# Performance work log

Measured on AMD Instinct MI355X. Metric: run time of the kernel, lower is better.

The kernel has to match this reference:

```python
import jax, jax.numpy as jnp
import numpy as np

TBL_V = 1000      # table_id_vocab
IDX_V = 100000    # idx_id_vocab
D     = 128       # embed_dim
T_OUT = 8         # output_length
BLK   = 2048      # block_size
H     = 8         # n_heads
L     = 2         # n_layers
DFF   = 2048      # nn.TransformerEncoderLayer default dim_feedforward
HID   = 4 * D     # hidden_dim
B, S  = 128, 200
NSEG  = IDX_V // BLK + 1   # 49 segment tables
EPS   = 1e-5


def setup_inputs() -> dict:
    key = jax.random.key(0)
    ks = iter(jax.random.split(key, 48))
    def n(shape, s=0.02):
        return jax.random.normal(next(ks), shape, jnp.float32) * s
    return {
        "table_id_seq": jax.random.randint(next(ks), (B, S), 0, TBL_V, jnp.int32),
        "idx_id_seq":   jax.random.randint(next(ks), (B, S), 0, IDX_V, jnp.int32),
        # embedding tables (idx tables stacked: segment s occupies rows [s*BLK,(s+1)*BLK))
        "table_embed": n((TBL_V, D), 1.0),
        "idx_embed":   n((NSEG * BLK, D), 1.0),
        # two independent TransformerEncoders (axis 0: 0=table, 1=idx), L layers each
        "Wqkv": n((2, L, 3 * D, D)), "bqkv": jnp.zeros((2, L, 3 * D), jnp.float32),
        "Wo":   n((2, L, D, D)),     "bo":   jnp.zeros((2, L, D), jnp.float32),
        "ln1_g": jnp.ones((2, L, D), jnp.float32), "ln1_b": jnp.zeros((2, L, D), jnp.float32),
        "W1": n((2, L, DFF, D)), "b1": jnp.zeros((2, L, DFF), jnp.float32),
        "W2": n((2, L, D, DFF)), "b2": jnp.zeros((2, L, D), jnp.float32),
        "ln2_g": jnp.ones((2, L, D), jnp.float32), "ln2_b": jnp.zeros((2, L, D), jnp.float32),
        "Wlin": n((HID, 2 * D)), "blin": jnp.zeros((HID,), jnp.float32),
        "Wtab": n((TBL_V, HID + 1)), "btab": jnp.zeros((TBL_V,), jnp.float32),
        "Widx": n((IDX_V, HID + 1)), "bidx": jnp.zeros((IDX_V,), jnp.float32),
    }


def _ln(x, g, b):
    m = x.mean(-1, keepdims=True)
    v = ((x - m) ** 2).mean(-1, keepdims=True)
    return (x - m) / jnp.sqrt(v + EPS) * g + b


def _encoder(x, p):
    """Post-norm TransformerEncoder (PyTorch defaults, eval mode). x: [B,S,D]."""
    Wqkv, bqkv, Wo, bo, g1, be1, W1, bf1, W2, bf2, g2, be2 = p
    Bz, Sl, Dm = x.shape
    hd = Dm // H
    for l in range(L):
        qkv = x @ Wqkv[l].T + bqkv[l]
        q, k, v = jnp.split(qkv, 3, axis=-1)
        q = q.reshape(Bz, Sl, H, hd)
        k = k.reshape(Bz, Sl, H, hd)
        v = v.reshape(Bz, Sl, H, hd)
        att = jnp.einsum('bqhd,bkhd->bhqk', q, k) * (hd ** -0.5)
        att = jax.nn.softmax(att, axis=-1)
        o = jnp.einsum('bhqk,bkhd->bqhd', att, v).reshape(Bz, Sl, Dm)
        o = o @ Wo[l].T + bo[l]
        x = _ln(x + o, g1[l], be1[l])
        f = jax.nn.relu(x @ W1[l].T + bf1[l]) @ W2[l].T + bf2[l]
        x = _ln(x + f, g2[l], be2[l])
    return x


def reference(table_id_seq, idx_id_seq, table_embed, idx_embed,
              Wqkv, bqkv, Wo, bo, ln1_g, ln1_b, W1, b1, W2, b2, ln2_g, ln2_b,
              Wlin, blin, Wtab, btab, Widx, bidx):
    enc_p = (Wqkv, bqkv, Wo, bo, ln1_g, ln1_b, W1, b1, W2, b2, ln2_g, ln2_b)
    te = table_embed[table_id_seq]                    # [B,S,D]
    # segment-routed lookup: row (seg*BLK + local) of stacked tables == original id
    ie = idx_embed[idx_id_seq]                        # [B,S,D]
    te = _encoder(te, tuple(a[0] for a in enc_p))
    ie = _encoder(ie, tuple(a[1] for a in enc_p))
    h = jnp.concatenate([te.mean(axis=1), ie.mean(axis=1)], axis=-1)  # mean over seq
    h = jax.nn.relu(h @ Wlin.T + blin)                # [B,HID]
    t = jnp.arange(T_OUT, dtype=h.dtype)
    # projection of [hidden, t]: base term + t * (last weight column)
    tab = (h @ Wtab[:, :HID].T + btab)[:, None, :] + t[None, :, None] * Wtab[:, HID][None, None, :]
    idx = (h @ Widx[:, :HID].T + bidx)[:, None, :] + t[None, :, None] * Widx[:, HID][None, None, :]
    return tab.reshape(-1, TBL_V), idx.reshape(-1, IDX_V)
```

## Files before the change

kernel.cpp:

```cpp
#include <hip/hip_runtime.h>

typedef __bf16 bf16x8 __attribute__((ext_vector_type(8)));
typedef float floatx4 __attribute__((ext_vector_type(4)));

__device__ __forceinline__ float u2f(unsigned short u) {
  union { unsigned int i; float f; } v; v.i = ((unsigned int)u) << 16; return v.f;
}
__device__ __forceinline__ unsigned short f2b(float f) {
  union { float f; unsigned int i; } v; v.f = f;
  unsigned int r = (v.i + 0x7fffu + ((v.i >> 16) & 1u)) >> 16;
  return (unsigned short)r;
}

__device__ __forceinline__ void gl16(const void* g, void* l) {
  __builtin_amdgcn_global_load_lds(
      (const __attribute__((address_space(1))) unsigned int*)g,
      (__attribute__((address_space(3))) unsigned int*)l, 16, 0, 0);
}

#define FCH 18048
#define QCH 8832
#define OCH 18176

#define LDS_STRIDE 48

__global__ __launch_bounds__(256) void gemm_kernel(
    const unsigned short* __restrict__ A, int lda,
    const float* __restrict__ W, int ldw,
    const float* __restrict__ bias,
    unsigned short* __restrict__ outB, float* __restrict__ outF,
    int M, int N, int K, int ldc, int mode)
{
  __shared__ unsigned short As[128 * LDS_STRIDE];
  __shared__ unsigned short Bs[128 * LDS_STRIDE];

  const int tid  = threadIdx.x;
  const int m0   = blockIdx.y * 128;
  const int n0   = blockIdx.x * 128;
  const int wave = tid >> 6;
  const int lane = tid & 63;
  const int wm   = (wave >> 1) * 64;
  const int wn   = (wave & 1) * 64;
  const int lr   = lane & 15;
  const int lq   = lane >> 4;

  floatx4 acc[4][4];
#pragma unroll
  for (int i = 0; i < 4; i++)
#pragma unroll
    for (int j = 0; j < 4; j++)
      acc[i][j] = (floatx4){0.f, 0.f, 0.f, 0.f};

  for (int k0 = 0; k0 < K; k0 += 32) {
    __syncthreads();
#pragma unroll
    for (int i = 0; i < 2; i++) {
      int c   = tid + i * 256;
      int row = c >> 2;
      int k8  = (c & 3) * 8;
      uint4 val = {0u, 0u, 0u, 0u};
      if (m0 + row < M)
        val = *(const uint4*)(A + (size_t)(m0 + row) * lda + k0 + k8);
      *(uint4*)(&As[row * LDS_STRIDE + k8]) = val;
    }
#pragma unroll
    for (int i = 0; i < 4; i++) {
      int c   = tid + i * 256;
      int row = c >> 3;
      int k4  = (c & 7) * 4;
      float f0 = 0.f, f1 = 0.f, f2 = 0.f, f3 = 0.f;
      if (n0 + row < N) {
        const float* p = W + (size_t)(n0 + row) * ldw + k0 + k4;
        f0 = p[0]; f1 = p[1]; f2 = p[2]; f3 = p[3];
      }
      ushort4 pk;
      pk.x = f2b(f0); pk.y = f2b(f1); pk.z = f2b(f2); pk.w = f2b(f3);
      *(ushort4*)(&Bs[row * LDS_STRIDE + k4]) = pk;
    }
    __syncthreads();

    bf16x8 af[4], bfr[4];
#pragma unroll
    for (int t = 0; t < 4; t++) {
      af[t]  = *(const bf16x8*)(&As[(wm + t * 16 + lr) * LDS_STRIDE + lq * 8]);
      bfr[t] = *(const bf16x8*)(&Bs[(wn + t * 16 + lr) * LDS_STRIDE + lq * 8]);
    }
#pragma unroll
    for (int tm = 0; tm < 4; tm++)
#pragma unroll
      for (int tn = 0; tn < 4; tn++)
        acc[tm][tn] = __builtin_amdgcn_mfma_f32_16x16x32_bf16(
            af[tm], bfr[tn], acc[tm][tn], 0, 0, 0);
  }

#pragma unroll
  for (int tm = 0; tm < 4; tm++) {
#pragma unroll
    for (int tn = 0; tn < 4; tn++) {
      int gcol = n0 + wn + tn * 16 + lr;
      if (gcol >= N) continue;
      float bs = bias[gcol];
      if (mode == 2) {
        float wl = W[(size_t)gcol * ldw + K];
#pragma unroll
        for (int r = 0; r < 4; r++) {
          int grow = m0 + wm + tm * 16 + lq * 4 + r;
          float base = acc[tm][tn][r] + bs;
          float* op = outF + ((size_t)grow * 8) * (size_t)N + gcol;
#pragma unroll
          for (int t = 0; t < 8; t++)
            op[(size_t)t * N] = base + (float)t * wl;
        }
      } else {
#pragma unroll
        for (int r = 0; r < 4; r++) {
          int grow = m0 + wm + tm * 16 + lq * 4 + r;
          if (grow < M) {
            float v = acc[tm][tn][r] + bs;
            if (mode == 1) v = fmaxf(v, 0.f);
            outB[(size_t)grow * ldc + gcol] = f2b(v);
          }
        }
      }
    }
  }
}

#define QKSTR 40
#define PSTR  232

__global__ __launch_bounds__(256) void attn_kernel(
    const unsigned short* __restrict__ qkv, unsigned short* __restrict__ out)
{
  __shared__ __attribute__((aligned(16))) unsigned short qsh[208 * QKSTR];
  __shared__ __attribute__((aligned(16))) unsigned short ksh[208 * QKSTR];
  __shared__ __attribute__((aligned(16))) unsigned short vsh[16 * PSTR];
  __shared__ __attribute__((aligned(16))) unsigned short psh[4][16 * PSTR];

  const int bh   = blockIdx.x;
  const int b    = bh >> 3, h = bh & 7;
  const int tid  = threadIdx.x;
  const int wave = tid >> 6;
  const int lane = tid & 63;
  const int lr   = lane & 15;
  const int lq   = lane >> 4;
  const size_t rowbase = (size_t)b * 200;

  for (int i = tid; i < 208 * QKSTR / 2; i += 256) {
    ((unsigned int*)qsh)[i] = 0u;
    ((unsigned int*)ksh)[i] = 0u;
  }
  for (int i = tid; i < 16 * PSTR / 2; i += 256)
    ((unsigned int*)vsh)[i] = 0u;
  for (int i = tid; i < 4 * 16 * PSTR / 2; i += 256)
    ((unsigned int*)&psh[0][0])[i] = 0u;
  __syncthreads();

  for (int i = tid; i < 800; i += 256) {
    int s = i >> 2, d4 = (i & 3) * 4;
    const unsigned short* base = qkv + (rowbase + s) * 384 + h * 16 + d4;
    uint2 qv = *(const uint2*)(base);
    uint2 kv = *(const uint2*)(base + 128);
    uint2 vv = *(const uint2*)(base + 256);
    *(uint2*)&qsh[s * QKSTR + d4] = qv;
    *(uint2*)&ksh[s * QKSTR + d4] = kv;
    vsh[(d4 + 0) * PSTR + s] = (unsigned short)(vv.x & 0xffffu);
    vsh[(d4 + 1) * PSTR + s] = (unsigned short)(vv.x >> 16);
    vsh[(d4 + 2) * PSTR + s] = (unsigned short)(vv.y & 0xffffu);
    vsh[(d4 + 3) * PSTR + s] = (unsigned short)(vv.y >> 16);
  }
  __syncthreads();

  unsigned short* pw = &psh[wave][0];

  for (int t = wave; t < 13; t += 4) {
    const int q0 = t * 16;
    bf16x8 qf = *(const bf16x8*)&qsh[(q0 + lr) * QKSTR + lq * 8];

    floatx4 s[13];
#pragma unroll
    for (int c = 0; c < 13; c++) {
      bf16x8 kf = *(const bf16x8*)&ksh[(c * 16 + lr) * QKSTR + lq * 8];
      s[c] = __builtin_amdgcn_mfma_f32_16x16x32_bf16(
          qf, kf, (floatx4){0.f, 0.f, 0.f, 0.f}, 0, 0, 0);
    }

    float mx[4] = {-1e30f, -1e30f, -1e30f, -1e30f};
#pragma unroll
    for (int c = 0; c < 13; c++)
#pragma unroll
      for (int r = 0; r < 4; r++) {
        float v = s[c][r] * 0.25f;
        if (c == 12 && lr >= 8) v = -1e30f;
        s[c][r] = v;
        mx[r] = fmaxf(mx[r], v);
      }
#pragma unroll
    for (int m = 1; m < 16; m <<= 1)
#pragma unroll
      for (int r = 0; r < 4; r++)
        mx[r] = fmaxf(mx[r], __shfl_xor(mx[r], m, 16));

    float sm[4] = {0.f, 0.f, 0.f, 0.f};
#pragma unroll
    for (int c = 0; c < 13; c++)
#pragma unroll
      for (int r = 0; r < 4; r++) {
        float e = __expf(s[c][r] - mx[r]);
        s[c][r] = e;
        sm[r] += e;
      }
#pragma unroll
    for (int m = 1; m < 16; m <<= 1)
#pragma unroll
      for (int r = 0; r < 4; r++)
        sm[r] += __shfl_xor(sm[r], m, 16);

#pragma unroll
    for (int c = 0; c < 13; c++)
#pragma unroll
      for (int r = 0; r < 4; r++)
        pw[(lq * 4 + r) * PSTR + c * 16 + lr] = f2b(s[c][r]);

    floatx4 o = {0.f, 0.f, 0.f, 0.f};
#pragma unroll
    for (int ks = 0; ks < 7; ks++) {
      bf16x8 pf = *(const bf16x8*)&pw[lr * PSTR + ks * 32 + lq * 8];
      bf16x8 vf = *(const bf16x8*)&vsh[lr * PSTR + ks * 32 + lq * 8];
      o = __builtin_amdgcn_mfma_f32_16x16x32_bf16(pf, vf, o, 0, 0, 0);
    }

#pragma unroll
    for (int r = 0; r < 4; r++) {
      int q = q0 + lq * 4 + r;
      if (q < 200)
        out[(rowbase + q) * 128 + h * 16 + lr] = f2b(o[r] / sm[r]);
    }
  }
}

__global__ __launch_bounds__(256) void prep_kernel(
    const float* __restrict__ W1, const float* __restrict__ b1,
    const float* __restrict__ W2,
    const float* __restrict__ Wqkv, const float* __restrict__ bqkv,
    const float* __restrict__ Wo, const float* __restrict__ bo,
    const float* __restrict__ ln1g, const float* __restrict__ ln1b,
    unsigned short* __restrict__ fimg, unsigned short* __restrict__ qimg,
    unsigned short* __restrict__ oimg)
{
  const int blk = blockIdx.x;
  const int tid = threadIdx.x;
  if (blk < 128) {
    const int pi = blk >> 5, c = blk & 31;
    unsigned short* o = fimg + (size_t)blk * FCH;
    const float* w1 = W1 + ((size_t)pi * 2048 + c * 64) * 128;
    const float* w2 = W2 + (size_t)pi * 128 * 2048 + c * 64;
    for (int u = tid; u < 64 * 34; u += 256) {
      int row = u / 34, c4 = (u % 34) * 4;
      ushort4 pk = {0, 0, 0, 0};
      if (c4 < 128) {
        const float* p = w1 + row * 128 + c4;
        pk.x = f2b(p[0]); pk.y = f2b(p[1]); pk.z = f2b(p[2]); pk.w = f2b(p[3]);
      }
      *(ushort4*)&o[row * 136 + c4] = pk;
    }
    for (int u = tid; u < 128 * 18; u += 256) {
      int row = u / 18, c4 = (u % 18) * 4;
      ushort4 pk = {0, 0, 0, 0};
      if (c4 < 64) {
        const float* p = w2 + (size_t)row * 2048 + c4;
        pk.x = f2b(p[0]); pk.y = f2b(p[1]); pk.z = f2b(p[2]); pk.w = f2b(p[3]);
      }
      *(ushort4*)&o[8704 + row * 72 + c4] = pk;
    }
    if (tid < 64)
      ((float*)(o + 17920))[tid] = b1[(size_t)pi * 2048 + c * 64 + tid];
  } else if (blk < 152) {
    const int q = blk - 128;
    const int pi = q / 6, c = q % 6;
    unsigned short* o = qimg + (size_t)q * QCH;
    const float* w = Wqkv + ((size_t)pi * 384 + c * 64) * 128;
    for (int u = tid; u < 64 * 34; u += 256) {
      int row = u / 34, c4 = (u % 34) * 4;
      ushort4 pk = {0, 0, 0, 0};
      if (c4 < 128) {
        const float* p = w + row * 128 + c4;
        pk.x = f2b(p[0]); pk.y = f2b(p[1]); pk.z = f2b(p[2]); pk.w = f2b(p[3]);
      }
      *(ushort4*)&o[row * 136 + c4] = pk;
    }
    if (tid < 64)
      ((float*)(o + 8704))[tid] = bqkv[(size_t)pi * 384 + c * 64 + tid];
  } else {
    const int pi = blk - 152;
    unsigned short* o = oimg + (size_t)pi * OCH;
    const float* w = Wo + (size_t)pi * 128 * 128;
    for (int u = tid; u < 128 * 34; u += 256) {
      int row = u / 34, c4 = (u % 34) * 4;
      ushort4 pk = {0, 0, 0, 0};
      if (c4 < 128) {
        const float* p = w + row * 128 + c4;
        pk.x = f2b(p[0]); pk.y = f2b(p[1]); pk.z = f2b(p[2]); pk.w = f2b(p[3]);
      }
      *(ushort4*)&o[row * 136 + c4] = pk;
    }
    if (tid < 128) {
      ((float*)(o + 17408))[tid] = bo[(size_t)pi * 128 + tid];
      ((float*)(o + 17664))[tid] = ln1g[(size_t)pi * 128 + tid];
      ((float*)(o + 17920))[tid] = ln1b[(size_t)pi * 128 + tid];
    }
  }
}

__global__ __launch_bounds__(256) void qkv_kernel(
    const unsigned short* __restrict__ x,
    const unsigned short* __restrict__ wimg,
    unsigned short* __restrict__ out)
{
  __shared__ __attribute__((aligned(16))) unsigned short wbuf[2][QCH];

  const int tid  = threadIdx.x;
  const int wave = tid >> 6;
  const int lane = tid & 63;
  const int lr   = lane & 15;
  const int lq   = lane >> 4;
  const int m0   = blockIdx.x * 64;
  const int wm   = wave * 16;

  bf16x8 af[4];
#pragma unroll
  for (int ks = 0; ks < 4; ks++)
    af[ks] = *(const bf16x8*)(x + (size_t)(m0 + wm + lr) * 128 + ks * 32 + lq * 8);

#pragma unroll
  for (int i = 0; i < 5; i++) {
    int u = tid + i * 256;
    if (u < 1104) gl16(wimg + (size_t)u * 8, &wbuf[0][(size_t)u * 8]);
  }

  for (int c = 0; c < 6; c++) {
    if (c + 1 < 6) {
      const unsigned short* src = wimg + (size_t)(c + 1) * QCH;
      unsigned short* dst = &wbuf[(c + 1) & 1][0];
#pragma unroll
      for (int i = 0; i < 5; i++) {
        int u = tid + i * 256;
        if (u < 1104) gl16(src + (size_t)u * 8, dst + (size_t)u * 8);
      }
      asm volatile("s_waitcnt vmcnt(5)" ::: "memory");
    } else {
      asm volatile("s_waitcnt vmcnt(0)" ::: "memory");
    }
    __builtin_amdgcn_s_barrier();
    __builtin_amdgcn_sched_barrier(0);

    const unsigned short* wb = &wbuf[c & 1][0];

    floatx4 acc[4];
#pragma unroll
    for (int tn = 0; tn < 4; tn++) acc[tn] = (floatx4){0.f, 0.f, 0.f, 0.f};
#pragma unroll
    for (int ks = 0; ks < 4; ks++)
#pragma unroll
      for (int tn = 0; tn < 4; tn++) {
        bf16x8 wf = *(const bf16x8*)&wb[(tn * 16 + lr) * 136 + ks * 32 + lq * 8];
        acc[tn] = __builtin_amdgcn_mfma_f32_16x16x32_bf16(af[ks], wf, acc[tn], 0, 0, 0);
      }
    const float* bc = (const float*)(wb + 8704);
#pragma unroll
    for (int tn = 0; tn < 4; tn++) {
      float bb = bc[tn * 16 + lr];
#pragma unroll
      for (int r = 0; r < 4; r++) {
        int row = m0 + wm + lq * 4 + r;
        out[(size_t)row * 384 + c * 64 + tn * 16 + lr] = f2b(acc[tn][r] + bb);
      }
    }
    __builtin_amdgcn_s_barrier();
  }
}

__global__ __launch_bounds__(256) void wo_ln_kernel(
    const unsigned short* __restrict__ attn,
    const unsigned short* __restrict__ wimg,
    unsigned short* __restrict__ x)
{
  __shared__ __attribute__((aligned(16))) unsigned short wbuf[OCH];

  const int tid  = threadIdx.x;
  const int wave = tid >> 6;
  const int lane = tid & 63;
  const int lr   = lane & 15;
  const int lq   = lane >> 4;
  const int m0   = blockIdx.x * 64;
  const int wm   = wave * 16;

#pragma unroll
  for (int i = 0; i < 9; i++) {
    int u = tid + i * 256;
    if (u < 2272) gl16(wimg + (size_t)u * 8, &wbuf[(size_t)u * 8]);
  }

  bf16x8 af[4];
#pragma unroll
  for (int ks = 0; ks < 4; ks++)
    af[ks] = *(const bf16x8*)(attn + (size_t)(m0 + wm + lr) * 128 + ks * 32 + lq * 8);

  asm volatile("s_waitcnt vmcnt(0)" ::: "memory");
  __builtin_amdgcn_s_barrier();
  __builtin_amdgcn_sched_barrier(0);

  floatx4 acc[8];
#pragma unroll
  for (int i = 0; i < 8; i++) acc[i] = (floatx4){0.f, 0.f, 0.f, 0.f};
#pragma unroll
  for (int ks = 0; ks < 4; ks++)
#pragma unroll
    for (int tn = 0; tn < 8; tn++) {
      bf16x8 wf = *(const bf16x8*)&wbuf[(tn * 16 + lr) * 136 + ks * 32 + lq * 8];
      acc[tn] = __builtin_amdgcn_mfma_f32_16x16x32_bf16(af[ks], wf, acc[tn], 0, 0, 0);
    }

  const float* bo = (const float*)(wbuf + 17408);
  const float* g  = (const float*)(wbuf + 17664);
  const float* bb = (const float*)(wbuf + 17920);

  float v[8][4];
  float s[4] = {0.f, 0.f, 0.f, 0.f}, ss[4] = {0.f, 0.f, 0.f, 0.f};
#pragma unroll
  for (int tn = 0; tn < 8; tn++) {
    float bsv = bo[tn * 16 + lr];
#pragma unroll
    for (int r = 0; r < 4; r++) {
      size_t idx = (size_t)(m0 + wm + lq * 4 + r) * 128 + tn * 16 + lr;
      float t = acc[tn][r] + bsv + u2f(x[idx]);
      v[tn][r] = t;
      s[r] += t;
      ss[r] += t * t;
    }
  }
#pragma unroll
  for (int m = 1; m < 16; m <<= 1)
#pragma unroll
    for (int r = 0; r < 4; r++) {
      s[r]  += __shfl_xor(s[r], m, 16);
      ss[r] += __shfl_xor(ss[r], m, 16);
    }
  float mean[4], rstd[4];
#pragma unroll
  for (int r = 0; r < 4; r++) {
    mean[r] = s[r] * (1.f / 128.f);
    float var = ss[r] * (1.f / 128.f) - mean[r] * mean[r];
    rstd[r] = rsqrtf(var + 1e-5f);
  }
#pragma unroll
  for (int tn = 0; tn < 8; tn++) {
    int col = tn * 16 + lr;
    float gv = g[col], bv = bb[col];
#pragma unroll
    for (int r = 0; r < 4; r++) {
      size_t idx = (size_t)(m0 + wm + lq * 4 + r) * 128 + col;
      x[idx] = f2b((v[tn][r] - mean[r]) * rstd[r] * gv + bv);
    }
  }
}

__global__ __launch_bounds__(256) void ffn_kernel(
    const unsigned short* __restrict__ xin,
    const unsigned short* __restrict__ wimg,
    const float* __restrict__ b2,
    const float* __restrict__ g2, const float* __restrict__ bb2,
    unsigned short* __restrict__ x)
{
  __shared__ __attribute__((aligned(16))) unsigned short wbuf[2][FCH];
  __shared__ __attribute__((aligned(16))) unsigned short mids[64 * 72];

  const int tid  = threadIdx.x;
  const int wave = tid >> 6;
  const int lane = tid & 63;
  const int lr   = lane & 15;
  const int lq   = lane >> 4;
  const int m0   = blockIdx.x * 64;
  const int wm   = wave * 16;

  bf16x8 af[4];
#pragma unroll
  for (int ks = 0; ks < 4; ks++)
    af[ks] = *(const bf16x8*)(xin + (size_t)(m0 + wm + lr) * 128 + ks * 32 + lq * 8);

  floatx4 acc[8];
#pragma unroll
  for (int i = 0; i < 8; i++) acc[i] = (floatx4){0.f, 0.f, 0.f, 0.f};

#pragma unroll
  for (int i = 0; i < 9; i++) {
    int u = tid + i * 256;
    if (u < 2256) gl16(wimg + (size_t)u * 8, &wbuf[0][(size_t)u * 8]);
  }

  for (int c = 0; c < 32; c++) {
    if (c + 1 < 32) {
      const unsigned short* src = wimg + (size_t)(c + 1) * FCH;
      unsigned short* dst = &wbuf[(c + 1) & 1][0];
#pragma unroll
      for (int i = 0; i < 9; i++) {
        int u = tid + i * 256;
        if (u < 2256) gl16(src + (size_t)u * 8, dst + (size_t)u * 8);
      }
      asm volatile("s_waitcnt vmcnt(9)" ::: "memory");
    } else {
      asm volatile("s_waitcnt vmcnt(0)" ::: "memory");
    }
    __builtin_amdgcn_s_barrier();
    __builtin_amdgcn_sched_barrier(0);

    const unsigned short* wb = &wbuf[c & 1][0];

    floatx4 macc[4];
#pragma unroll
    for (int tn = 0; tn < 4; tn++) macc[tn] = (floatx4){0.f, 0.f, 0.f, 0.f};
#pragma unroll
    for (int ks = 0; ks < 4; ks++)
#pragma unroll
      for (int tn = 0; tn < 4; tn++) {
        bf16x8 wf = *(const bf16x8*)&wb[(tn * 16 + lr) * 136 + ks * 32 + lq * 8];
        macc[tn] = __builtin_amdgcn_mfma_f32_16x16x32_bf16(af[ks], wf, macc[tn], 0, 0, 0);
      }
    const float* b1c = (const float*)(wb + 17920);
#pragma unroll
    for (int tn = 0; tn < 4; tn++) {
      float bb = b1c[tn * 16 + lr];
#pragma unroll
      for (int r = 0; r < 4; r++) {
        float v = fmaxf(macc[tn][r] + bb, 0.f);
        mids[(wm + lq * 4 + r) * 72 + tn * 16 + lr] = f2b(v);
      }
    }
#pragma unroll
    for (int ks = 0; ks < 2; ks++) {
      bf16x8 mf = *(const bf16x8*)&mids[(wm + lr) * 72 + ks * 32 + lq * 8];
#pragma unroll
      for (int tn = 0; tn < 8; tn++) {
        bf16x8 wf = *(const bf16x8*)&wb[8704 + (tn * 16 + lr) * 72 + ks * 32 + lq * 8];
        acc[tn] = __builtin_amdgcn_mfma_f32_16x16x32_bf16(mf, wf, acc[tn], 0, 0, 0);
      }
    }
    __builtin_amdgcn_s_barrier();
  }

  float v[8][4];
  float s[4] = {0.f, 0.f, 0.f, 0.f}, ss[4] = {0.f, 0.f, 0.f, 0.f};
#pragma unroll
  for (int tn = 0; tn < 8; tn++) {
    float bsv = b2[tn * 16 + lr];
#pragma unroll
    for (int r = 0; r < 4; r++) {
      size_t idx = (size_t)(m0 + wm + lq * 4 + r) * 128 + tn * 16 + lr;
      float t = acc[tn][r] + bsv + u2f(x[idx]);
      v[tn][r] = t;
      s[r] += t;
      ss[r] += t * t;
    }
  }
#pragma unroll
  for (int m = 1; m < 16; m <<= 1)
#pragma unroll
    for (int r = 0; r < 4; r++) {
      s[r]  += __shfl_xor(s[r], m, 16);
      ss[r] += __shfl_xor(ss[r], m, 16);
    }
  float mean[4], rstd[4];
#pragma unroll
  for (int r = 0; r < 4; r++) {
    mean[r] = s[r] * (1.f / 128.f);
    float var = ss[r] * (1.f / 128.f) - mean[r] * mean[r];
    rstd[r] = rsqrtf(var + 1e-5f);
  }
#pragma unroll
  for (int tn = 0; tn < 8; tn++) {
    int col = tn * 16 + lr;
    float gv = g2[col], bv = bb2[col];
#pragma unroll
    for (int r = 0; r < 4; r++) {
      size_t idx = (size_t)(m0 + wm + lq * 4 + r) * 128 + col;
      x[idx] = f2b((v[tn][r] - mean[r]) * rstd[r] * gv + bv);
    }
  }
}

__global__ __launch_bounds__(256) void gather_kernel(
    const int* __restrict__ ids, const float* __restrict__ table,
    unsigned short* __restrict__ x)
{
  int t0 = blockIdx.x * 256 + threadIdx.x;
#pragma unroll
  for (int i = 0; i < 4; i++) {
    int u = t0 + i * 409600;
    int row = u >> 6, dp = (u & 63) << 1;
    int id = ids[row];
    const float* p = table + (size_t)id * 128 + dp;
    float f0 = p[0], f1 = p[1];
    ((unsigned int*)x)[u] = (unsigned int)f2b(f0) | ((unsigned int)f2b(f1) << 16);
  }
}

__global__ __launch_bounds__(512) void pool_kernel(
    const unsigned short* __restrict__ x, unsigned short* __restrict__ hcat,
    int col0)
{
  __shared__ float part[512];
  int b = blockIdx.x;
  int d = threadIdx.x & 127;
  int g = threadIdx.x >> 7;
  float s = 0.f;
  for (int t = 0; t < 50; t++)
    s += u2f(x[(size_t)(b * 200 + g * 50 + t) * 128 + d]);
  part[threadIdx.x] = s;
  __syncthreads();
  if (g == 0) {
    float tot = part[d] + part[d + 128] + part[d + 256] + part[d + 384];
    hcat[b * 256 + col0 + d] = f2b(tot * (1.f / 200.f));
  }
}

static void gemm(hipStream_t st, const unsigned short* A, int lda,
                 const float* W, int ldw, const float* bias,
                 unsigned short* outB, float* outF,
                 int M, int N, int K, int ldc, int mode)
{
  dim3 grid((N + 127) / 128, (M + 127) / 128);
  gemm_kernel<<<grid, dim3(256), 0, st>>>(A, lda, W, ldw, bias, outB, outF,
                                          M, N, K, ldc, mode);
}

extern "C" void kernel_launch(void* const* d_in, const int* in_sizes, int n_in,
                              void* d_out, int out_size, void* d_ws, size_t ws_size,
                              hipStream_t stream)
{
  const int*   tab_ids     = (const int*)d_in[0];
  const int*   idx_ids     = (const int*)d_in[1];
  const float* table_embed = (const float*)d_in[2];
  const float* idx_embed   = (const float*)d_in[3];
  const float* Wqkv = (const float*)d_in[4];
  const float* bqkv = (const float*)d_in[5];
  const float* Wo   = (const float*)d_in[6];
  const float* bo   = (const float*)d_in[7];
  const float* ln1g = (const float*)d_in[8];
  const float* ln1b = (const float*)d_in[9];
  const float* W1   = (const float*)d_in[10];
  const float* b1   = (const float*)d_in[11];
  const float* W2   = (const float*)d_in[12];
  const float* b2   = (const float*)d_in[13];
  const float* ln2g = (const float*)d_in[14];
  const float* ln2b = (const float*)d_in[15];
  const float* Wlin = (const float*)d_in[16];
  const float* blin = (const float*)d_in[17];
  const float* Wtab = (const float*)d_in[18];
  const float* btab = (const float*)d_in[19];
  const float* Widx = (const float*)d_in[20];
  const float* bidx = (const float*)d_in[21];
  float* out = (float*)d_out;
  char*  ws  = (char*)d_ws;

  const size_t off_x    = 0;
  const size_t off_qkv  = 6553600;
  const size_t off_attn = 26214400;
  const size_t off_hcat = 32768000;
  const size_t off_h    = off_hcat + 65536;
  const size_t off_fimg = 33030144;
  const size_t off_qimg = off_fimg + (size_t)128 * FCH * 2;
  const size_t off_oimg = off_qimg + (size_t)24 * QCH * 2;

  unsigned short* x    = (unsigned short*)(ws + off_x);
  unsigned short* qkv  = (unsigned short*)(ws + off_qkv);
  unsigned short* attn = (unsigned short*)(ws + off_attn);
  unsigned short* hcat = (unsigned short*)(ws + off_hcat);
  unsigned short* h    = (unsigned short*)(ws + off_h);
  unsigned short* fimg = (unsigned short*)(ws + off_fimg);
  unsigned short* qimg = (unsigned short*)(ws + off_qimg);
  unsigned short* oimg = (unsigned short*)(ws + off_oimg);

  prep_kernel<<<156, 256, 0, stream>>>(W1, b1, W2, Wqkv, bqkv, Wo, bo,
                                       ln1g, ln1b, fimg, qimg, oimg);

  for (int e = 0; e < 2; e++) {
    gather_kernel<<<1600, 256, 0, stream>>>(
        e == 0 ? tab_ids : idx_ids,
        e == 0 ? table_embed : idx_embed, x);
    for (int l = 0; l < 2; l++) {
      int pi = e * 2 + l;
      qkv_kernel<<<400, 256, 0, stream>>>(x, qimg + (size_t)pi * 6 * QCH, qkv);
      attn_kernel<<<1024, 256, 0, stream>>>(qkv, attn);
      wo_ln_kernel<<<400, 256, 0, stream>>>(attn, oimg + (size_t)pi * OCH, x);
      ffn_kernel<<<400, 256, 0, stream>>>(
          x, fimg + (size_t)pi * 32 * FCH, b2 + pi * 128,
          ln2g + pi * 128, ln2b + pi * 128, x);
    }
    pool_kernel<<<128, 512, 0, stream>>>(x, hcat, e * 128);
  }

  gemm(stream, hcat, 256, Wlin, 256, blin, h, nullptr, 128, 512, 256, 512, 1);
  gemm(stream, h, 512, Wtab, 513, btab, nullptr, out,           128, 1000,   512, 1000,   2);
  gemm(stream, h, 512, Widx, 513, bidx, nullptr, out + 1024000, 128, 100000, 512, 100000, 2);
}
```

Measured before the change: 1.296 ms.

## Halve FFN weight chunk to 32 columns and trim attention LDS zeroing

The FFN kernel now streams the hidden dimension in 64 chunks of 32 instead of 32 chunks of 64. This shrinks the per-chunk LDS image and the mids buffer, which lowers LDS use per block and can raise occupancy. Chunk sizes are padded to 10240 elements so every thread loads exactly five 16-byte pieces and the bounds checks go away. The attention kernel now zeroes only the padding regions instead of clearing all shared buffers, which also removes one barrier. The trade-off is twice as many chunk iterations and barriers in the FFN, with less MFMA work in each.

```diff
diff --git a/kernel.cpp b/kernel.cpp
--- a/kernel.cpp
+++ b/kernel.cpp
@@ -18,8 +18,8 @@
       (__attribute__((address_space(3))) unsigned int*)l, 16, 0, 0);
 }
 
-#define FCH 18048
-#define QCH 8832
+#define FCH 10240
+#define QCH 10240
 #define OCH 18176
 
 #define LDS_STRIDE 48
@@ -146,16 +146,25 @@
   const int lq   = lane >> 4;
   const size_t rowbase = (size_t)b * 200;
 
-  for (int i = tid; i < 208 * QKSTR / 2; i += 256) {
-    ((unsigned int*)qsh)[i] = 0u;
-    ((unsigned int*)ksh)[i] = 0u;
-  }
-  for (int i = tid; i < 16 * PSTR / 2; i += 256)
-    ((unsigned int*)vsh)[i] = 0u;
-  for (int i = tid; i < 4 * 16 * PSTR / 2; i += 256)
-    ((unsigned int*)&psh[0][0])[i] = 0u;
-  __syncthreads();
-
+  {
+    int rem = tid & 127;
+    int row = 200 + (rem >> 4);
+    int col = (rem & 15) * 2;
+    unsigned int* dst = (tid < 128) ? (unsigned int*)&qsh[row * QKSTR + col]
+                                    : (unsigned int*)&ksh[row * QKSTR + col];
+    *dst = 0u;
+  }
+  {
+    int row = tid >> 4, col = 200 + (tid & 15) * 2;
+    *(unsigned int*)&vsh[row * PSTR + col] = 0u;
+  }
+  for (int u = tid; u < 512; u += 256) {
+    int w = u >> 7, rem = u & 127;
+    int row = rem >> 3, col = 208 + (rem & 7) * 2;
+    *(unsigned int*)&psh[w][row * PSTR + col] = 0u;
+  }
+
+  const uint2 z2 = {0u, 0u};
   for (int i = tid; i < 800; i += 256) {
     int s = i >> 2, d4 = (i & 3) * 4;
     const unsigned short* base = qkv + (rowbase + s) * 384 + h * 16 + d4;
@@ -164,6 +173,8 @@
     uint2 vv = *(const uint2*)(base + 256);
     *(uint2*)&qsh[s * QKSTR + d4] = qv;
     *(uint2*)&ksh[s * QKSTR + d4] = kv;
+    *(uint2*)&qsh[s * QKSTR + 16 + d4] = z2;
+    *(uint2*)&ksh[s * QKSTR + 16 + d4] = z2;
     vsh[(d4 + 0) * PSTR + s] = (unsigned short)(vv.x & 0xffffu);
     vsh[(d4 + 1) * PSTR + s] = (unsigned short)(vv.x >> 16);
     vsh[(d4 + 2) * PSTR + s] = (unsigned short)(vv.y & 0xffffu);
@@ -250,12 +261,12 @@
 {
   const int blk = blockIdx.x;
   const int tid = threadIdx.x;
-  if (blk < 128) {
-    const int pi = blk >> 5, c = blk & 31;
+  if (blk < 256) {
+    const int pi = blk >> 6, c = blk & 63;
     unsigned short* o = fimg + (size_t)blk * FCH;
-    const float* w1 = W1 + ((size_t)pi * 2048 + c * 64) * 128;
-    const float* w2 = W2 + (size_t)pi * 128 * 2048 + c * 64;
-    for (int u = tid; u < 64 * 34; u += 256) {
+    const float* w1 = W1 + ((size_t)pi * 2048 + c * 32) * 128;
+    const float* w2 = W2 + (size_t)pi * 128 * 2048 + c * 32;
+    for (int u = tid; u < 32 * 34; u += 256) {
       int row = u / 34, c4 = (u % 34) * 4;
       ushort4 pk = {0, 0, 0, 0};
       if (c4 < 128) {
@@ -264,19 +275,19 @@
       }
       *(ushort4*)&o[row * 136 + c4] = pk;
     }
-    for (int u = tid; u < 128 * 18; u += 256) {
-      int row = u / 18, c4 = (u % 18) * 4;
+    for (int u = tid; u < 128 * 10; u += 256) {
+      int row = u / 10, c4 = (u % 10) * 4;
       ushort4 pk = {0, 0, 0, 0};
-      if (c4 < 64) {
+      if (c4 < 32) {
         const float* p = w2 + (size_t)row * 2048 + c4;
         pk.x = f2b(p[0]); pk.y = f2b(p[1]); pk.z = f2b(p[2]); pk.w = f2b(p[3]);
       }
-      *(ushort4*)&o[8704 + row * 72 + c4] = pk;
-    }
-    if (tid < 64)
-      ((float*)(o + 17920))[tid] = b1[(size_t)pi * 2048 + c * 64 + tid];
-  } else if (blk < 152) {
-    const int q = blk - 128;
+      *(ushort4*)&o[4352 + row * 40 + c4] = pk;
+    }
+    if (tid < 32)
+      ((float*)(o + 9472))[tid] = b1[(size_t)pi * 2048 + c * 32 + tid];
+  } else if (blk < 280) {
+    const int q = blk - 256;
     const int pi = q / 6, c = q % 6;
     unsigned short* o = qimg + (size_t)q * QCH;
     const float* w = Wqkv + ((size_t)pi * 384 + c * 64) * 128;
@@ -292,7 +303,7 @@
     if (tid < 64)
       ((float*)(o + 8704))[tid] = bqkv[(size_t)pi * 384 + c * 64 + tid];
   } else {
-    const int pi = blk - 152;
+    const int pi = blk - 280;
     unsigned short* o = oimg + (size_t)pi * OCH;
     const float* w = Wo + (size_t)pi * 128 * 128;
     for (int u = tid; u < 128 * 34; u += 256) {
@@ -335,7 +346,7 @@
 #pragma unroll
   for (int i = 0; i < 5; i++) {
     int u = tid + i * 256;
-    if (u < 1104) gl16(wimg + (size_t)u * 8, &wbuf[0][(size_t)u * 8]);
+    gl16(wimg + (size_t)u * 8, &wbuf[0][(size_t)u * 8]);
   }
 
   for (int c = 0; c < 6; c++) {
@@ -345,7 +356,7 @@
 #pragma unroll
       for (int i = 0; i < 5; i++) {
         int u = tid + i * 256;
-        if (u < 1104) gl16(src + (size_t)u * 8, dst + (size_t)u * 8);
+        gl16(src + (size_t)u * 8, dst + (size_t)u * 8);
       }
       asm volatile("s_waitcnt vmcnt(5)" ::: "memory");
     } else {
@@ -473,7 +484,7 @@
     unsigned short* __restrict__ x)
 {
   __shared__ __attribute__((aligned(16))) unsigned short wbuf[2][FCH];
-  __shared__ __attribute__((aligned(16))) unsigned short mids[64 * 72];
+  __shared__ __attribute__((aligned(16))) unsigned short mids[64 * 40];
 
   const int tid  = threadIdx.x;
   const int wave = tid >> 6;
@@ -493,21 +504,21 @@
   for (int i = 0; i < 8; i++) acc[i] = (floatx4){0.f, 0.f, 0.f, 0.f};
 
 #pragma unroll
-  for (int i = 0; i < 9; i++) {
+  for (int i = 0; i < 5; i++) {
     int u = tid + i * 256;
-    if (u < 2256) gl16(wimg + (size_t)u * 8, &wbuf[0][(size_t)u * 8]);
-  }
-
-  for (int c = 0; c < 32; c++) {
-    if (c + 1 < 32) {
+    gl16(wimg + (size_t)u * 8, &wbuf[0][(size_t)u * 8]);
+  }
+
+  for (int c = 0; c < 64; c++) {
+    if (c + 1 < 64) {
       const unsigned short* src = wimg + (size_t)(c + 1) * FCH;
       unsigned short* dst = &wbuf[(c + 1) & 1][0];
 #pragma unroll
-      for (int i = 0; i < 9; i++) {
+      for (int i = 0; i < 5; i++) {
         int u = tid + i * 256;
-        if (u < 2256) gl16(src + (size_t)u * 8, dst + (size_t)u * 8);
-      }
-      asm volatile("s_waitcnt vmcnt(9)" ::: "memory");
+        gl16(src + (size_t)u * 8, dst + (size_t)u * 8);
+      }
+      asm volatile("s_waitcnt vmcnt(5)" ::: "memory");
     } else {
       asm volatile("s_waitcnt vmcnt(0)" ::: "memory");
     }
@@ -516,32 +527,31 @@
 
     const unsigned short* wb = &wbuf[c & 1][0];
 
-    floatx4 macc[4];
-#pragma unroll
-    for (int tn = 0; tn < 4; tn++) macc[tn] = (floatx4){0.f, 0.f, 0.f, 0.f};
+    floatx4 macc[2];
+#pragma unroll
+    for (int tn = 0; tn < 2; tn++) macc[tn] = (floatx4){0.f, 0.f, 0.f, 0.f};
 #pragma unroll
     for (int ks = 0; ks < 4; ks++)
 #pragma unroll
-      for (int tn = 0; tn < 4; tn++) {
+      for (int tn = 0; tn < 2; tn++) {
         bf16x8 wf = *(const bf16x8*)&wb[(tn * 16 + lr) * 136 + ks * 32 + lq * 8];
         macc[tn] = __builtin_amdgcn_mfma_f32_16x16x32_bf16(af[ks], wf, macc[tn], 0, 0, 0);
       }
-    const float* b1c = (const float*)(wb + 17920);
-#pragma unroll
-    for (int tn = 0; tn < 4; tn++) {
+    const float* b1c = (const float*)(wb + 9472);
+#pragma unroll
+    for (int tn = 0; tn < 2; tn++) {
       float bb = b1c[tn * 16 + lr];
 #pragma unroll
       for (int r = 0; r < 4; r++) {
         float v = fmaxf(macc[tn][r] + bb, 0.f);
-        mids[(wm + lq * 4 + r) * 72 + tn * 16 + lr] = f2b(v);
-      }
-    }
-#pragma unroll
-    for (int ks = 0; ks < 2; ks++) {
-      bf16x8 mf = *(const bf16x8*)&mids[(wm + lr) * 72 + ks * 32 + lq * 8];
+        mids[(wm + lq * 4 + r) * 40 + tn * 16 + lr] = f2b(v);
+      }
+    }
+    {
+      bf16x8 mf = *(const bf16x8*)&mids[(wm + lr) * 40 + lq * 8];
 #pragma unroll
       for (int tn = 0; tn < 8; tn++) {
-        bf16x8 wf = *(const bf16x8*)&wb[8704 + (tn * 16 + lr) * 72 + ks * 32 + lq * 8];
+        bf16x8 wf = *(const bf16x8*)&wb[4352 + (tn * 16 + lr) * 40 + lq * 8];
         acc[tn] = __builtin_amdgcn_mfma_f32_16x16x32_bf16(mf, wf, acc[tn], 0, 0, 0);
       }
     }
@@ -668,7 +678,7 @@
   const size_t off_hcat = 32768000;
   const size_t off_h    = off_hcat + 65536;
   const size_t off_fimg = 33030144;
-  const size_t off_qimg = off_fimg + (size_t)128 * FCH * 2;
+  const size_t off_qimg = off_fimg + (size_t)256 * FCH * 2;
   const size_t off_oimg = off_qimg + (size_t)24 * QCH * 2;
 
   unsigned short* x    = (unsigned short*)(ws + off_x);
@@ -680,7 +690,7 @@
   unsigned short* qimg = (unsigned short*)(ws + off_qimg);
   unsigned short* oimg = (unsigned short*)(ws + off_oimg);
 
-  prep_kernel<<<156, 256, 0, stream>>>(W1, b1, W2, Wqkv, bqkv, Wo, bo,
+  prep_kernel<<<284, 256, 0, stream>>>(W1, b1, W2, Wqkv, bqkv, Wo, bo,
                                        ln1g, ln1b, fimg, qimg, oimg);
 
   for (int e = 0; e < 2; e++) {
@@ -693,7 +703,7 @@
       attn_kernel<<<1024, 256, 0, stream>>>(qkv, attn);
       wo_ln_kernel<<<400, 256, 0, stream>>>(attn, oimg + (size_t)pi * OCH, x);
       ffn_kernel<<<400, 256, 0, stream>>>(
-          x, fimg + (size_t)pi * 32 * FCH, b2 + pi * 128,
+          x, fimg + (size_t)pi * 64 * FCH, b2 + pi * 128,
           ln2g + pi * 128, ln2b + pi * 128, x);
     }
     pool_kernel<<<128, 512, 0, stream>>>(x, hcat, e * 128);
```

After: 1.340 ms. 1.03x slower.
